# Performance work log

Measured on AMD Instinct MI355X. Metric: run time of the kernel, lower is better.

Reference implementation:

```python
import jax, jax.numpy as jnp
import numpy as np

EMBED_DIM = 2048
NUM_HEADS = 32
NUM_KV_HEADS = 8
HEAD_DIM = EMBED_DIM // NUM_HEADS          # 64
GROUP = NUM_HEADS // NUM_KV_HEADS          # 4 queries per KV head
BATCH, SEQ = 2, 2048


def setup_inputs() -> dict:
    key = jax.random.key(0)
    ks = jax.random.split(key, 9)
    s_in = 1.0 / np.sqrt(EMBED_DIM)
    kv_dim = NUM_KV_HEADS * HEAD_DIM
    return {
        "x":      jax.random.normal(ks[0], (BATCH, SEQ, EMBED_DIM), jnp.float32),
        "Wq":     jax.random.normal(ks[1], (EMBED_DIM, EMBED_DIM), jnp.float32) * s_in,
        "bq":     jnp.zeros((EMBED_DIM,), jnp.float32),
        "Wk":     jax.random.normal(ks[2], (EMBED_DIM, kv_dim), jnp.float32) * s_in,
        "bk":     jnp.zeros((kv_dim,), jnp.float32),
        "Wv":     jax.random.normal(ks[3], (EMBED_DIM, kv_dim), jnp.float32) * s_in,
        "bv":     jnp.zeros((kv_dim,), jnp.float32),
        "Wo":     jax.random.normal(ks[4], (EMBED_DIM, EMBED_DIM), jnp.float32) * s_in,
        "bo":     jnp.zeros((EMBED_DIM,), jnp.float32),
    }


def reference(x, Wq, bq, Wk, bk, Wv, bv, Wo, bo):
    B, S, _ = x.shape
    # Projections (torch Linear == x @ W + b with W stored as [in, out] here)
    q = (x @ Wq + bq).reshape(B, S, NUM_KV_HEADS, GROUP, HEAD_DIM)  # grouped heads
    k = (x @ Wk + bk).reshape(B, S, NUM_KV_HEADS, HEAD_DIM)
    v = (x @ Wv + bv).reshape(B, S, NUM_KV_HEADS, HEAD_DIM)

    scale = 1.0 / np.sqrt(HEAD_DIM)
    # scores[b, h, g, s, t] = q[b, s, h, g, :] . k[b, t, h, :]
    # (repeat_interleave of K across the group dim == broadcasting over g)
    scores = jnp.einsum("bshgd,bthd->bhgst", q, k) * scale
    attn = jax.nn.softmax(scores, axis=-1)
    out = jnp.einsum("bhgst,bthd->bshgd", attn, v)  # [B, S, kvh, g, D]
    out = out.reshape(B, S, EMBED_DIM)
    return out @ Wo + bo
```

## Files before the change

kernel.cpp:

```cpp
#include <hip/hip_runtime.h>


typedef __attribute__((ext_vector_type(8)))  short     s16x8;
typedef __attribute__((ext_vector_type(8)))  _Float16  h8;
typedef __attribute__((ext_vector_type(2)))  __fp16    fp16x2;
typedef __attribute__((ext_vector_type(4)))  float     f32x4;
typedef __attribute__((ext_vector_type(16))) float     f32x16;

#define DEVI static __device__ __forceinline__

#if __has_builtin(__builtin_amdgcn_exp2f)
#define EXP2F __builtin_amdgcn_exp2f
#else
#define EXP2F exp2f
#endif

DEVI short f2h(float f){ _Float16 h = (_Float16)f; return __builtin_bit_cast(short, h); }
DEVI unsigned pkh(float a, float b){
  fp16x2 t = __builtin_amdgcn_cvt_pkrtz(a, b);
  return __builtin_bit_cast(unsigned, t);
}

typedef __attribute__((address_space(3))) unsigned       lds_u32;
typedef __attribute__((address_space(1))) const unsigned gbl_u32;
DEVI void glds16(const short* g, short* l){
  __builtin_amdgcn_global_load_lds((gbl_u32*)g, (lds_u32*)l, 16, 0, 0);
}

__global__ void cast_kernel(const float* __restrict__ in, short* __restrict__ out, int n){
  int i = (blockIdx.x * 256 + threadIdx.x) * 8;
  if(i >= n) return;
  float4 a = *(const float4*)(in + i);
  float4 b = *(const float4*)(in + i + 4);
  s16x8 v;
  v[0]=f2h(a.x); v[1]=f2h(a.y); v[2]=f2h(a.z); v[3]=f2h(a.w);
  v[4]=f2h(b.x); v[5]=f2h(b.y); v[6]=f2h(b.z); v[7]=f2h(b.w);
  *(s16x8*)(out + i) = v;
}

__global__ void prep_kernel(const float* __restrict__ Wq, const float* __restrict__ Wk,
                            const float* __restrict__ Wv, const float* __restrict__ Wo,
                            const float* __restrict__ bq, const float* __restrict__ bk,
                            const float* __restrict__ bv,
                            short* __restrict__ WT, short* __restrict__ WoT,
                            float* __restrict__ bqkv){
  __shared__ __align__(16) short tile[64*72];
  const int gy = blockIdx.y;
  const int t = threadIdx.x;
  if(gy >= 80){
    int i = blockIdx.x * 256 + t;
    if(i < 3072) bqkv[i] = (i < 2048) ? bq[i] : (i < 2560 ? bk[i-2048] : bv[i-2560]);
    return;
  }
  const float* src; short* dst; int ldin, by;
  if(gy < 32)      { src = Wq; dst = WT;             ldin = 2048; by = gy;    }
  else if(gy < 40) { src = Wk; dst = WT + 2048*2048; ldin =  512; by = gy-32; }
  else if(gy < 48) { src = Wv; dst = WT + 2560*2048; ldin =  512; by = gy-40; }
  else             { src = Wo; dst = WoT;            ldin = 2048; by = gy-48; }
  const int tr = blockIdx.x * 64;
  const int tc = by * 64;
  for(int c = t; c < 512; c += 256){
    int r = c >> 3, g = c & 7;
    const float* p = src + (size_t)(tr + r) * ldin + tc + g*8;
    s16x8 v;
    #pragma unroll
    for(int e = 0; e < 8; e++) v[e] = f2h(p[e]);
    *(s16x8*)&tile[r*72 + g*8] = v;
  }
  __syncthreads();
  for(int c = t; c < 512; c += 256){
    int r = c >> 3, g = c & 7;
    s16x8 v;
    #pragma unroll
    for(int e = 0; e < 8; e++) v[e] = tile[(g*8+e)*72 + r];
    *(s16x8*)(dst + (size_t)(tc + r) * 2048 + tr + g*8) = v;
  }
}

template<bool OUT_F32>
__global__ __launch_bounds__(256, 2)
void gemm_bt_kernel(const short* __restrict__ A, const short* __restrict__ BT,
                    const float* __restrict__ bias, void* __restrict__ C,
                    int M, int N, int K, int scale_cols, float qscale){
  __shared__ __align__(16) short As[128*32];
  __shared__ __align__(16) short Bs[128*32];
  const int m0 = blockIdx.x * 128;
  const int n0 = blockIdx.y * 128;
  const int tid = threadIdx.x;
  const int wave = tid >> 6, lane = tid & 63;
  const int l16 = lane & 15, quad = lane >> 4;
  const int wm = (wave >> 1) * 64, wn = (wave & 1) * 64;

  const short* gA = A  + (size_t)(m0 + wave*32 + (lane>>2))*K + (lane&3)*8;
  const short* gB = BT + (size_t)(n0 + wave*32 + (lane>>2))*K + (lane&3)*8;
  short* lA = As + wave*32*32;
  short* lB = Bs + wave*32*32;

  f32x4 acc[4][4];
  #pragma unroll
  for(int i=0;i<4;i++)
    #pragma unroll
    for(int j=0;j<4;j++) acc[i][j] = (f32x4)(0.0f);

  for(int k0 = 0; k0 < K; k0 += 32){
    glds16(gA + k0,                lA);
    glds16(gA + 16*(size_t)K + k0, lA + 512);
    glds16(gB + k0,                lB);
    glds16(gB + 16*(size_t)K + k0, lB + 512);
    __syncthreads();
    h8 af[4], bfr[4];
    #pragma unroll
    for(int i=0;i<4;i++){
      af[i]  = *(const h8*)&As[(wm + i*16 + l16)*32 + quad*8];
      bfr[i] = *(const h8*)&Bs[(wn + i*16 + l16)*32 + quad*8];
    }
    #pragma unroll
    for(int i=0;i<4;i++)
      #pragma unroll
      for(int j=0;j<4;j++)
        acc[i][j] = __builtin_amdgcn_mfma_f32_16x16x32_f16(af[i], bfr[j], acc[i][j], 0, 0, 0);
    __syncthreads();
  }

  #pragma unroll
  for(int j=0;j<4;j++){
    int col = n0 + wn + j*16 + l16;
    float bb = bias[col];
    float sc = (col < scale_cols) ? qscale : 1.0f;
    #pragma unroll
    for(int i=0;i<4;i++){
      #pragma unroll
      for(int r=0;r<4;r++){
        size_t row = (size_t)(m0 + wm + i*16 + quad*4 + r);
        float v = (acc[i][j][r] + bb) * sc;
        if(OUT_F32) ((float*)C)[row*(size_t)N + col] = v;
        else        ((short*)C)[row*(size_t)N + col] = f2h(v);
      }
    }
  }
}

__global__ void fragpack_kernel(const short* __restrict__ QKV,
                                short* __restrict__ Kf, short* __restrict__ Vf){
  __shared__ __align__(16) short kt[64*72];
  __shared__ __align__(16) short vt[64*72];
  const int t = blockIdx.x, kvh = blockIdx.y, b = blockIdx.z;
  const int tid = threadIdx.x;
  const size_t rowbase = (size_t)(b*2048 + t*64);
  for(int c = tid; c < 512; c += 256){
    int r = c >> 3, g = c & 7;
    const short* src = QKV + (rowbase + r)*3072 + kvh*64 + g*8;
    *(s16x8*)&kt[r*72 + g*8] = *(const s16x8*)(src + 2048);
    *(s16x8*)&vt[r*72 + g*8] = *(const s16x8*)(src + 2560);
  }
  __syncthreads();
  const size_t obase = ((size_t)(b*8 + kvh)*32 + t) * 4096;
  for(int ch = tid; ch < 512; ch += 256){
    int kb = ch >> 8, l = ch & 63;
    int c = l & 31, h = l >> 5;
    int ks2 = (ch >> 6) & 3;
    *(s16x8*)(Kf + obase + (size_t)ch*8) =
        *(const s16x8*)&kt[(kb*32 + c)*72 + ks2*16 + h*8];
    int ksp = (ch >> 7) & 1, mb = (ch >> 6) & 1;
    int k0 = kb*32 + ksp*16 + h*4;
    int d  = mb*32 + c;
    s16x8 v;
    #pragma unroll
    for(int j = 0; j < 4; j++){
      v[j]   = vt[(k0 + j)*72 + d];
      v[4+j] = vt[(k0 + 8 + j)*72 + d];
    }
    *(s16x8*)(Vf + obase + (size_t)ch*8) = v;
  }
}

__global__ __launch_bounds__(256, 2)
void attn_kernel(const short* __restrict__ Qg, const short* __restrict__ Kf,
                 const short* __restrict__ Vf, short* __restrict__ Og, int ldq){
  const int L = blockIdx.x;
  const int nid = (L & 7)*64 + (L >> 3);
  const int qt  = nid & 31;
  const int grp = nid >> 5;
  const int kvh = grp & 7, b = grp >> 3;
  const int tid = threadIdx.x;
  const int wave = tid >> 6, lane = tid & 63;
  const int c = lane & 31, h = lane >> 5;
  const int head = kvh*4 + wave;
  const int q0 = qt * 64;

  h8 qreg[4][2];
  #pragma unroll
  for(int ks2=0; ks2<4; ks2++)
    #pragma unroll
    for(int qg=0; qg<2; qg++)
      qreg[ks2][qg] = *(const h8*)(Qg + (size_t)(b*2048 + q0 + qg*32 + c)*ldq
                                      + head*64 + ks2*16 + h*8);

  float lsum[2] = {0.0f, 0.0f};
  f32x16 oacc[2][2];
  #pragma unroll
  for(int qg=0; qg<2; qg++)
    #pragma unroll
    for(int mb=0; mb<2; mb++) oacc[qg][mb] = (f32x16)(0.0f);

  const short* kp = Kf + (size_t)grp * 131072 + lane*8;
  const short* vp = Vf + (size_t)grp * 131072 + lane*8;

  h8 kA[4], vA[4], kB[4], vB[4];

  auto loadf = [&](size_t it, h8* K, h8* V){
    const short* kq = kp + it*2048;
    const short* vq = vp + it*2048;
    #pragma unroll
    for(int i=0;i<4;i++){
      K[i] = *(const h8*)(kq + i*512);
      V[i] = *(const h8*)(vq + i*512);
    }
  };

  auto compute = [&](const h8* K, const h8* V){
    f32x16 st[2];
    st[0] = (f32x16)(0.0f); st[1] = (f32x16)(0.0f);
    #pragma unroll
    for(int ks2=0; ks2<4; ks2++){
      st[0] = __builtin_amdgcn_mfma_f32_32x32x16_f16(K[ks2], qreg[ks2][0], st[0], 0, 0, 0);
      st[1] = __builtin_amdgcn_mfma_f32_32x32x16_f16(K[ks2], qreg[ks2][1], st[1], 0, 0, 0);
    }
    union H8U { h8 v; unsigned u[4]; };
    H8U pk[2][2];
    #pragma unroll
    for(int qg=0; qg<2; qg++){
      float sacc = 0.0f;
      #pragma unroll
      for(int j=0; j<4; j++){
        float pa = EXP2F(st[qg][2*j]);
        float pb = EXP2F(st[qg][2*j+1]);
        sacc += pa + pb;
        pk[qg][0].u[j] = pkh(pa, pb);
      }
      #pragma unroll
      for(int j=0; j<4; j++){
        float pa = EXP2F(st[qg][8+2*j]);
        float pb = EXP2F(st[qg][8+2*j+1]);
        sacc += pa + pb;
        pk[qg][1].u[j] = pkh(pa, pb);
      }
      lsum[qg] += sacc;
    }
    #pragma unroll
    for(int ksp=0; ksp<2; ksp++){
      #pragma unroll
      for(int mb=0; mb<2; mb++){
        oacc[0][mb] = __builtin_amdgcn_mfma_f32_32x32x16_f16(V[ksp*2+mb], pk[0][ksp].v, oacc[0][mb], 0, 0, 0);
        oacc[1][mb] = __builtin_amdgcn_mfma_f32_32x32x16_f16(V[ksp*2+mb], pk[1][ksp].v, oacc[1][mb], 0, 0, 0);
      }
    }
  };

  loadf(0, kA, vA);
  #pragma unroll 1
  for(int it = 0; it < 64; it += 2){
    loadf((size_t)(it+1), kB, vB);
    compute(kA, vA);
    loadf((size_t)(it+2 < 64 ? it+2 : 0), kA, vA);
    compute(kB, vB);
  }

  #pragma unroll
  for(int qg=0; qg<2; qg++){
    lsum[qg] += __shfl_xor(lsum[qg], 32);
    float li = 1.0f / lsum[qg];
    size_t rowoff = (size_t)(b*2048 + q0 + qg*32 + c)*2048 + head*64;
    #pragma unroll
    for(int mb=0; mb<2; mb++){
      #pragma unroll
      for(int g2=0; g2<4; g2++){
        int d0 = mb*32 + 8*g2 + 4*h;
        uint2 wv;
        wv.x = pkh(oacc[qg][mb][4*g2+0]*li, oacc[qg][mb][4*g2+1]*li);
        wv.y = pkh(oacc[qg][mb][4*g2+2]*li, oacc[qg][mb][4*g2+3]*li);
        *(uint2*)&Og[rowoff + d0] = wv;
      }
    }
  }
}

extern "C" void kernel_launch(void* const* d_in, const int* in_sizes, int n_in,
                              void* d_out, int out_size, void* d_ws, size_t ws_size,
                              hipStream_t stream){
  const float* x  = (const float*)d_in[0];
  const float* Wq = (const float*)d_in[1];
  const float* bq = (const float*)d_in[2];
  const float* Wk = (const float*)d_in[3];
  const float* bk = (const float*)d_in[4];
  const float* Wv = (const float*)d_in[5];
  const float* bv = (const float*)d_in[6];
  const float* Wo = (const float*)d_in[7];
  const float* bo = (const float*)d_in[8];

  char* ws = (char*)d_ws;
  short* WT   = (short*)(ws);
  short* WoT  = (short*)(ws + 25165824);
  short* xb   = (short*)(ws + 33554432);
  short* QKV  = (short*)(ws + 50331648);
  float* bqkv = (float*)(ws + 79691776);
  short* AO   = xb;
  short* Kf   = (short*)(ws);
  short* Vf   = (short*)(ws + 4194304);

  cast_kernel<<<4096, 256, 0, stream>>>(x, xb, 8388608);
  prep_kernel<<<dim3(32,81), 256, 0, stream>>>(Wq, Wk, Wv, Wo, bq, bk, bv, WT, WoT, bqkv);

  gemm_bt_kernel<false><<<dim3(32,24), 256, 0, stream>>>(xb, WT, bqkv, QKV,
                                                         4096, 3072, 2048,
                                                         2048, 0.1803368801111244f);

  fragpack_kernel<<<dim3(32,8,2), 256, 0, stream>>>(QKV, Kf, Vf);

  attn_kernel<<<512, 256, 0, stream>>>(QKV, Kf, Vf, AO, 3072);

  gemm_bt_kernel<true><<<dim3(32,16), 256, 0, stream>>>(AO, WoT, bo, (float*)d_out,
                                                        4096, 2048, 2048, 0, 1.0f);
}
```

Baseline: 317.2 us.

## Software-pipeline QK of next tile with softmax/PV of current tile, add setprio

Restructures the attention inner loop so the QK^T MFMAs for the next KV tile are issued before the exp/softmax and PV MFMAs of the current tile. K and V loads are split and issued separately so each buffer is refilled as soon as it is consumed. MFMA blocks are wrapped in s_setprio to favour matrix issue across waves. The aim is to overlap the transcendental softmax work with matrix-core work. The cost is more live registers (two score and two packed-P buffers), which may lower occupancy or cause spills.

```diff
diff --git a/kernel.cpp b/kernel.cpp
--- a/kernel.cpp
+++ b/kernel.cpp
@@ -207,27 +207,33 @@
   const short* vp = Vf + (size_t)grp * 131072 + lane*8;
 
   h8 kA[4], vA[4], kB[4], vB[4];
-
-  auto loadf = [&](size_t it, h8* K, h8* V){
+  f32x16 stA[2], stB[2];
+  union H8U { h8 v; unsigned u[4]; };
+  H8U pkA[2][2], pkB[2][2];
+
+  auto loadk = [&](size_t it, h8* K){
     const short* kq = kp + it*2048;
+    #pragma unroll
+    for(int i=0;i<4;i++) K[i] = *(const h8*)(kq + i*512);
+  };
+  auto loadv = [&](size_t it, h8* V){
     const short* vq = vp + it*2048;
     #pragma unroll
-    for(int i=0;i<4;i++){
-      K[i] = *(const h8*)(kq + i*512);
-      V[i] = *(const h8*)(vq + i*512);
-    }
-  };
-
-  auto compute = [&](const h8* K, const h8* V){
-    f32x16 st[2];
+    for(int i=0;i<4;i++) V[i] = *(const h8*)(vq + i*512);
+  };
+
+  auto qk = [&](const h8* K, f32x16* st){
     st[0] = (f32x16)(0.0f); st[1] = (f32x16)(0.0f);
+    __builtin_amdgcn_s_setprio(1);
     #pragma unroll
     for(int ks2=0; ks2<4; ks2++){
       st[0] = __builtin_amdgcn_mfma_f32_32x32x16_f16(K[ks2], qreg[ks2][0], st[0], 0, 0, 0);
       st[1] = __builtin_amdgcn_mfma_f32_32x32x16_f16(K[ks2], qreg[ks2][1], st[1], 0, 0, 0);
     }
-    union H8U { h8 v; unsigned u[4]; };
-    H8U pk[2][2];
+    __builtin_amdgcn_s_setprio(0);
+  };
+
+  auto sm = [&](const f32x16* st, H8U pk[2][2]){
     #pragma unroll
     for(int qg=0; qg<2; qg++){
       float sacc = 0.0f;
@@ -247,6 +253,10 @@
       }
       lsum[qg] += sacc;
     }
+  };
+
+  auto pv = [&](const h8* V, H8U pk[2][2]){
+    __builtin_amdgcn_s_setprio(1);
     #pragma unroll
     for(int ksp=0; ksp<2; ksp++){
       #pragma unroll
@@ -255,15 +265,27 @@
         oacc[1][mb] = __builtin_amdgcn_mfma_f32_32x32x16_f16(V[ksp*2+mb], pk[1][ksp].v, oacc[1][mb], 0, 0, 0);
       }
     }
-  };
-
-  loadf(0, kA, vA);
+    __builtin_amdgcn_s_setprio(0);
+  };
+
+  loadk(0, kA); loadv(0, vA);
+  loadk(1, kB); loadv(1, vB);
+  qk(kA, stA);
+
   #pragma unroll 1
   for(int it = 0; it < 64; it += 2){
-    loadf((size_t)(it+1), kB, vB);
-    compute(kA, vA);
-    loadf((size_t)(it+2 < 64 ? it+2 : 0), kA, vA);
-    compute(kB, vB);
+    const size_t i2 = (it+2 < 64) ? (size_t)(it+2) : 0;
+    const size_t i3 = (it+3 < 64) ? (size_t)(it+3) : 0;
+    qk(kB, stB);
+    loadk(i2, kA);
+    sm(stA, pkA);
+    pv(vA, pkA);
+    loadv(i2, vA);
+    qk(kA, stA);
+    loadk(i3, kB);
+    sm(stB, pkB);
+    pv(vB, pkB);
+    loadv(i3, vB);
   }
 
   #pragma unroll
```

After: 401.1 us. 26.5% more time.

## Software-pipeline QK of next tile with softmax/PV of current tile in attention

Applied to the files above, without the earlier changes.

Restructures the attention inner loop so the QK^T MFMAs for the next KV tile are issued before the exp/softmax and PV MFMAs of the current tile. K and V loads are staggered so each buffer is refilled right after its last use. s_setprio is raised around the MFMA blocks so matrix work from this wave gets issue priority over other waves' exp work. The aim is to overlap the transcendental VALU work with matrix-core work and to hide global load latency. In exchange it holds two score tiles live at once, which raises register pressure.

```diff
diff --git a/kernel.cpp b/kernel.cpp
--- a/kernel.cpp
+++ b/kernel.cpp
@@ -196,7 +196,7 @@
       qreg[ks2][qg] = *(const h8*)(Qg + (size_t)(b*2048 + q0 + qg*32 + c)*ldq
                                       + head*64 + ks2*16 + h*8);
 
-  float lsum[2] = {0.0f, 0.0f};
+  float lsum0 = 0.0f, lsum1 = 0.0f;
   f32x16 oacc[2][2];
   #pragma unroll
   for(int qg=0; qg<2; qg++)
@@ -206,70 +206,94 @@
   const short* kp = Kf + (size_t)grp * 131072 + lane*8;
   const short* vp = Vf + (size_t)grp * 131072 + lane*8;
 
-  h8 kA[4], vA[4], kB[4], vB[4];
-
-  auto loadf = [&](size_t it, h8* K, h8* V){
-    const short* kq = kp + it*2048;
-    const short* vq = vp + it*2048;
-    #pragma unroll
-    for(int i=0;i<4;i++){
-      K[i] = *(const h8*)(kq + i*512);
-      V[i] = *(const h8*)(vq + i*512);
-    }
-  };
-
-  auto compute = [&](const h8* K, const h8* V){
-    f32x16 st[2];
-    st[0] = (f32x16)(0.0f); st[1] = (f32x16)(0.0f);
-    #pragma unroll
-    for(int ks2=0; ks2<4; ks2++){
-      st[0] = __builtin_amdgcn_mfma_f32_32x32x16_f16(K[ks2], qreg[ks2][0], st[0], 0, 0, 0);
-      st[1] = __builtin_amdgcn_mfma_f32_32x32x16_f16(K[ks2], qreg[ks2][1], st[1], 0, 0, 0);
-    }
-    union H8U { h8 v; unsigned u[4]; };
-    H8U pk[2][2];
-    #pragma unroll
-    for(int qg=0; qg<2; qg++){
-      float sacc = 0.0f;
-      #pragma unroll
-      for(int j=0; j<4; j++){
-        float pa = EXP2F(st[qg][2*j]);
-        float pb = EXP2F(st[qg][2*j+1]);
-        sacc += pa + pb;
-        pk[qg][0].u[j] = pkh(pa, pb);
-      }
-      #pragma unroll
-      for(int j=0; j<4; j++){
-        float pa = EXP2F(st[qg][8+2*j]);
-        float pb = EXP2F(st[qg][8+2*j+1]);
-        sacc += pa + pb;
-        pk[qg][1].u[j] = pkh(pa, pb);
-      }
-      lsum[qg] += sacc;
-    }
-    #pragma unroll
-    for(int ksp=0; ksp<2; ksp++){
-      #pragma unroll
-      for(int mb=0; mb<2; mb++){
-        oacc[0][mb] = __builtin_amdgcn_mfma_f32_32x32x16_f16(V[ksp*2+mb], pk[0][ksp].v, oacc[0][mb], 0, 0, 0);
-        oacc[1][mb] = __builtin_amdgcn_mfma_f32_32x32x16_f16(V[ksp*2+mb], pk[1][ksp].v, oacc[1][mb], 0, 0, 0);
-      }
-    }
-  };
-
-  loadf(0, kA, vA);
+  h8 kA0, kA1, kA2, kA3;
+  h8 vA0, vA1, vA2, vA3;
+  f32x16 stA0, stA1, stB0, stB1;
+  union H8U { h8 v; unsigned u[4]; };
+  H8U pk00, pk01, pk10, pk11;
+
+#define LOADK(IT) do{ const short* kq_ = kp + (size_t)(IT)*2048;              \
+    kA0 = *(const h8*)(kq_);       kA1 = *(const h8*)(kq_ + 512);             \
+    kA2 = *(const h8*)(kq_ + 1024); kA3 = *(const h8*)(kq_ + 1536); }while(0)
+
+#define LOADV(IT) do{ const short* vq_ = vp + (size_t)(IT)*2048;              \
+    vA0 = *(const h8*)(vq_);       vA1 = *(const h8*)(vq_ + 512);             \
+    vA2 = *(const h8*)(vq_ + 1024); vA3 = *(const h8*)(vq_ + 1536); }while(0)
+
+#define QK_STEP(S0, S1) do{                                                   \
+    __builtin_amdgcn_s_setprio(1);                                            \
+    S0 = (f32x16)(0.0f); S1 = (f32x16)(0.0f);                                 \
+    S0 = __builtin_amdgcn_mfma_f32_32x32x16_f16(kA0, qreg[0][0], S0, 0,0,0);  \
+    S1 = __builtin_amdgcn_mfma_f32_32x32x16_f16(kA0, qreg[0][1], S1, 0,0,0);  \
+    S0 = __builtin_amdgcn_mfma_f32_32x32x16_f16(kA1, qreg[1][0], S0, 0,0,0);  \
+    S1 = __builtin_amdgcn_mfma_f32_32x32x16_f16(kA1, qreg[1][1], S1, 0,0,0);  \
+    S0 = __builtin_amdgcn_mfma_f32_32x32x16_f16(kA2, qreg[2][0], S0, 0,0,0);  \
+    S1 = __builtin_amdgcn_mfma_f32_32x32x16_f16(kA2, qreg[2][1], S1, 0,0,0);  \
+    S0 = __builtin_amdgcn_mfma_f32_32x32x16_f16(kA3, qreg[3][0], S0, 0,0,0);  \
+    S1 = __builtin_amdgcn_mfma_f32_32x32x16_f16(kA3, qreg[3][1], S1, 0,0,0);  \
+    __builtin_amdgcn_s_setprio(0); }while(0)
+
+#define SM_STEP(S0, S1) do{                                                   \
+    float sa0 = 0.0f, sa1 = 0.0f;                                             \
+    _Pragma("unroll")                                                         \
+    for(int j=0; j<4; j++){                                                   \
+      float a0 = EXP2F(S0[2*j]),   b0 = EXP2F(S0[2*j+1]);                     \
+      float a1 = EXP2F(S1[2*j]),   b1 = EXP2F(S1[2*j+1]);                     \
+      sa0 += a0 + b0; pk00.u[j] = pkh(a0, b0);                                \
+      sa1 += a1 + b1; pk10.u[j] = pkh(a1, b1);                                \
+    }                                                                         \
+    _Pragma("unroll")                                                         \
+    for(int j=0; j<4; j++){                                                   \
+      float a0 = EXP2F(S0[8+2*j]), b0 = EXP2F(S0[8+2*j+1]);                   \
+      float a1 = EXP2F(S1[8+2*j]), b1 = EXP2F(S1[8+2*j+1]);                   \
+      sa0 += a0 + b0; pk01.u[j] = pkh(a0, b0);                                \
+      sa1 += a1 + b1; pk11.u[j] = pkh(a1, b1);                                \
+    }                                                                         \
+    lsum0 += sa0; lsum1 += sa1; }while(0)
+
+#define PV_STEP() do{                                                         \
+    __builtin_amdgcn_s_setprio(1);                                            \
+    oacc[0][0] = __builtin_amdgcn_mfma_f32_32x32x16_f16(vA0, pk00.v, oacc[0][0], 0,0,0); \
+    oacc[1][0] = __builtin_amdgcn_mfma_f32_32x32x16_f16(vA0, pk10.v, oacc[1][0], 0,0,0); \
+    oacc[0][1] = __builtin_amdgcn_mfma_f32_32x32x16_f16(vA1, pk00.v, oacc[0][1], 0,0,0); \
+    oacc[1][1] = __builtin_amdgcn_mfma_f32_32x32x16_f16(vA1, pk10.v, oacc[1][1], 0,0,0); \
+    oacc[0][0] = __builtin_amdgcn_mfma_f32_32x32x16_f16(vA2, pk01.v, oacc[0][0], 0,0,0); \
+    oacc[1][0] = __builtin_amdgcn_mfma_f32_32x32x16_f16(vA2, pk11.v, oacc[1][0], 0,0,0); \
+    oacc[0][1] = __builtin_amdgcn_mfma_f32_32x32x16_f16(vA3, pk01.v, oacc[0][1], 0,0,0); \
+    oacc[1][1] = __builtin_amdgcn_mfma_f32_32x32x16_f16(vA3, pk11.v, oacc[1][1], 0,0,0); \
+    __builtin_amdgcn_s_setprio(0); }while(0)
+
+  LOADK(0); LOADV(0);
+  QK_STEP(stA0, stA1);
+  LOADK(1);
+
   #pragma unroll 1
   for(int it = 0; it < 64; it += 2){
-    loadf((size_t)(it+1), kB, vB);
-    compute(kA, vA);
-    loadf((size_t)(it+2 < 64 ? it+2 : 0), kA, vA);
-    compute(kB, vB);
-  }
+    const int i2 = (it+2 < 64) ? it+2 : 0;
+    const int i3 = (it+3 < 64) ? it+3 : 0;
+    QK_STEP(stB0, stB1);
+    LOADK(i2);
+    SM_STEP(stA0, stA1);
+    PV_STEP();
+    LOADV(it+1);
+    QK_STEP(stA0, stA1);
+    LOADK(i3);
+    SM_STEP(stB0, stB1);
+    PV_STEP();
+    LOADV(i2);
+  }
+
+#undef LOADK
+#undef LOADV
+#undef QK_STEP
+#undef SM_STEP
+#undef PV_STEP
 
   #pragma unroll
   for(int qg=0; qg<2; qg++){
-    lsum[qg] += __shfl_xor(lsum[qg], 32);
-    float li = 1.0f / lsum[qg];
+    float ls = (qg == 0) ? lsum0 : lsum1;
+    ls += __shfl_xor(ls, 32);
+    float li = 1.0f / ls;
     size_t rowoff = (size_t)(b*2048 + q0 + qg*32 + c)*2048 + head*64;
     #pragma unroll
     for(int mb=0; mb<2; mb++){
```

Result: slower. 372.0 us (+17.3%).
